# Kernel tuning notes

Measured on AMD Instinct MI355X. Metric: run time of the kernel, lower is better.

Reference implementation:

```python
import jax, jax.numpy as jnp
import numpy as np

D_MODEL = 1024
NUM_HEADS = 16
HEAD_DIM = D_MODEL // NUM_HEADS


def setup_inputs() -> dict:
    key = jax.random.key(0)
    ks = jax.random.split(key, 11)
    B, S = 2, 2048
    s = 1.0 / np.sqrt(D_MODEL)
    inp = {
        'q': jax.random.normal(ks[0], (B, S, D_MODEL), jnp.float32),
        'k': jax.random.normal(ks[1], (B, S, D_MODEL), jnp.float32),
        'v': jax.random.normal(ks[2], (B, S, D_MODEL), jnp.float32),
        'wq': jax.random.normal(ks[3], (D_MODEL, D_MODEL), jnp.float32) * s,
        'bq': jnp.zeros((D_MODEL,), jnp.float32),
        'wk': jax.random.normal(ks[4], (D_MODEL, D_MODEL), jnp.float32) * s,
        'bk': jnp.zeros((D_MODEL,), jnp.float32),
        'wv': jax.random.normal(ks[5], (D_MODEL, D_MODEL), jnp.float32) * s,
        'bv': jnp.zeros((D_MODEL,), jnp.float32),
        'wo': jax.random.normal(ks[6], (D_MODEL, D_MODEL), jnp.float32) * s,
        'bo': jnp.zeros((D_MODEL,), jnp.float32),
    }
    return inp


def _split_heads(x, B):
    # [B, S, D] -> [B, H, S, Hd]
    return x.reshape(B, -1, NUM_HEADS, HEAD_DIM).transpose(0, 2, 1, 3)


def reference(q, k, v, wq, bq, wk, bk, wv, bv, wo, bo):
    B = q.shape[0]
    qh = _split_heads(q @ wq + bq, B)
    kh = _split_heads(k @ wk + bk, B)
    vh = _split_heads(v @ wv + bv, B)
    scale = 1.0 / np.sqrt(HEAD_DIM).astype(np.float32)
    # [B, H, Sq, Sk]
    scores = jnp.einsum('bhqd,bhkd->bhqk', qh, kh) * scale
    probs = jax.nn.softmax(scores, axis=-1)
    out = jnp.einsum('bhqk,bhkd->bhqd', probs, vh)  # [B, H, Sq, Hd]
    out = out.transpose(0, 2, 1, 3).reshape(B, -1, D_MODEL)
    return out @ wo + bo
```

## Files before the change

kernel.cpp:

```cpp
#include <hip/hip_runtime.h>

typedef unsigned short u16;
typedef __bf16 bf16x8 __attribute__((ext_vector_type(8)));
typedef float    f32x4 __attribute__((ext_vector_type(4)));
typedef float   f32x16 __attribute__((ext_vector_type(16)));
typedef u16      u16x8 __attribute__((ext_vector_type(8)));
typedef u16      u16x4 __attribute__((ext_vector_type(4)));
typedef unsigned uint4v __attribute__((ext_vector_type(4)));

#define DM 1024
#define SQ 2048
#define HD 64
#define QSCALE 0.18033688f

#define SWZ8(row, ch) ((((ch) ^ ((row) & 7) ^ ((row) >> 3)) & 7))

__device__ __forceinline__ u16 f2bf(float f) {
    unsigned u = __builtin_bit_cast(unsigned, f);
    u += 0x7FFFu + ((u >> 16) & 1u);
    return (u16)(u >> 16);
}

__device__ __forceinline__ bf16x8 ldsbf(const u16* p) {
    return __builtin_bit_cast(bf16x8, *(const u16x8*)p);
}

__device__ __forceinline__ unsigned cvtpk(float a, float b) {
    unsigned r;
    asm("v_cvt_pk_bf16_f32 %0, %1, %2" : "=v"(r) : "v"(a), "v"(b));
    return r;
}

__device__ __forceinline__ void swap32(unsigned &a, unsigned &b) {
    asm volatile("v_permlane32_swap_b32 %0, %1" : "+v"(a), "+v"(b));
}

typedef __attribute__((address_space(3))) unsigned lds_u32_t;
typedef __attribute__((address_space(1))) const unsigned glob_u32_t;
__device__ __forceinline__ void gl_lds16(const u16* g, u16* l) {
    __builtin_amdgcn_global_load_lds((glob_u32_t*)g, (lds_u32_t*)l, 16, 0, 0);
}

__global__ __launch_bounds__(256) void convert_kernel(
    const float* __restrict__ q, const float* __restrict__ k,
    const float* __restrict__ v,
    u16* __restrict__ Qc, u16* __restrict__ Kc, u16* __restrict__ Vc)
{
    const int which = blockIdx.x >> 11;
    const float* src = (which==0) ? q : (which==1) ? k : v;
    u16* dst         = (which==0) ? Qc : (which==1) ? Kc : Vc;
    const int off = ((blockIdx.x & 2047) << 11) + threadIdx.x * 8;
    f32x4 x0 = *(const f32x4*)&src[off];
    f32x4 x1 = *(const f32x4*)&src[off + 4];
    u16x8 u;
#pragma unroll
    for (int e = 0; e < 4; ++e) { u[e] = f2bf(x0[e]); u[e+4] = f2bf(x1[e]); }
    *(u16x8*)&dst[off] = u;
}

__global__ __launch_bounds__(256) void wtrans_kernel(
    const float* __restrict__ w0, const float* __restrict__ w1,
    const float* __restrict__ w2, const float* __restrict__ w3,
    u16* __restrict__ t0, u16* __restrict__ t1,
    u16* __restrict__ t2, u16* __restrict__ t3)
{
    __shared__ float tile[32][33];
    const int z = blockIdx.z;
    const float* W = (z==0) ? w0 : (z==1) ? w1 : (z==2) ? w2 : w3;
    u16* T        = (z==0) ? t0 : (z==1) ? t1 : (z==2) ? t2 : t3;
    const float sc = (z==0) ? QSCALE : 1.0f;
    const int tx = threadIdx.x & 31, ty = threadIdx.x >> 5;
    const int n0 = blockIdx.x * 32, k0 = blockIdx.y * 32;
#pragma unroll
    for (int i = 0; i < 4; ++i)
        tile[ty + 8*i][tx] = W[(size_t)(k0 + ty + 8*i)*DM + n0 + tx];
    __syncthreads();
#pragma unroll
    for (int i = 0; i < 4; ++i)
        T[(size_t)(n0 + ty + 8*i)*DM + k0 + tx] = f2bf(tile[tx][ty + 8*i] * sc);
}

template<bool OF32, bool VTLAST>
__global__ __launch_bounds__(256) void gemm_kernel(
    const u16* __restrict__ a0, const u16* __restrict__ a1, const u16* __restrict__ a2,
    const u16* __restrict__ w0, const u16* __restrict__ w1, const u16* __restrict__ w2,
    const float* __restrict__ bi0, const float* __restrict__ bi1, const float* __restrict__ bi2,
    void* __restrict__ o0, void* __restrict__ o1, void* __restrict__ o2,
    float bscale0)
{
    __shared__ __align__(16) u16 As[128*64];
    __shared__ __align__(16) u16 Bs[128*64];

    const int cpx  = gridDim.x >> 3;
    const int wgid = (blockIdx.x & 7) * cpx + (blockIdx.x >> 3);
    const int z   = wgid >> 8;
    const int rem = wgid & 255;
    const int by  = rem >> 3, bx = rem & 7;

    const u16*  Ap  = (z==0) ? a0 : (z==1) ? a1 : a2;
    const u16*  Wp  = (z==0) ? w0 : (z==1) ? w1 : w2;
    const float* Bp = (z==0) ? bi0 : (z==1) ? bi1 : bi2;
    void* Op        = (z==0) ? o0 : (z==1) ? o1 : o2;
    const float bsc = (z==0) ? bscale0 : 1.0f;

    const int tid  = threadIdx.x;
    const int lane = tid & 63;
    const int wv   = tid >> 6;
    const int m0 = by * 128;
    const int n0 = bx * 128;
    const int wr = (wv >> 1) * 64;
    const int wc = (wv & 1) * 64;
    const int g  = lane >> 4;
    const int mm = lane & 15;

    const int l8  = lane >> 3;
    const int chs = (lane & 7) ^ l8;
    const int lrow = wv*8 + l8;

    const f32x4 zero4 = {0.f, 0.f, 0.f, 0.f};
    f32x4 acc[4][4];
#pragma unroll
    for (int i = 0; i < 4; ++i)
#pragma unroll
        for (int j = 0; j < 4; ++j) acc[i][j] = zero4;

    for (int kt = 0; kt < 16; ++kt) {
        const int k0 = kt * 64;
#pragma unroll
        for (int i = 0; i < 4; ++i) {
            const int row = i*32 + lrow;
            gl_lds16(&Ap[(size_t)(m0+row)*DM + k0 + chs*8], &As[(i*32 + wv*8)*64]);
            gl_lds16(&Wp[(size_t)(n0+row)*DM + k0 + chs*8], &Bs[(i*32 + wv*8)*64]);
        }
        __syncthreads();
#pragma unroll
        for (int ks = 0; ks < 2; ++ks) {
            bf16x8 af[4], bfr[4];
#pragma unroll
            for (int rt = 0; rt < 4; ++rt) {
                const int row = wr + rt*16 + mm;
                const int ch  = ks*4 + g;
                af[rt] = ldsbf(&As[row*64 + ((ch ^ (row & 7)) << 3)]);
            }
#pragma unroll
            for (int ct = 0; ct < 4; ++ct) {
                const int row = wc + ct*16 + mm;
                const int ch  = ks*4 + g;
                bfr[ct] = ldsbf(&Bs[row*64 + ((ch ^ (row & 7)) << 3)]);
            }
            __builtin_amdgcn_s_setprio(1);
#pragma unroll
            for (int rt = 0; rt < 4; ++rt)
#pragma unroll
                for (int ct = 0; ct < 4; ++ct)
                    acc[rt][ct] = __builtin_amdgcn_mfma_f32_16x16x32_bf16(
                        af[rt], bfr[ct], acc[rt][ct], 0, 0, 0);
            __builtin_amdgcn_s_setprio(0);
        }
        __syncthreads();
    }
    if (VTLAST && z == 2) {
#pragma unroll
        for (int ct = 0; ct < 4; ++ct) {
            const int col = n0 + wc + ct*16 + mm;
            const float bv = Bp[col] * bsc;
#pragma unroll
            for (int rt = 0; rt < 4; ++rt) {
                const int row0 = m0 + wr + rt*16 + g*4;
                const int bb = row0 >> 11, s = row0 & (SQ-1);
                u16x4 pk;
#pragma unroll
                for (int r = 0; r < 4; ++r) pk[r] = f2bf(acc[rt][ct][r] + bv);
                *(u16x4*)&((u16*)Op)[(size_t)(bb*DM + col)*SQ + s] = pk;
            }
        }
    } else {
#pragma unroll
        for (int ct = 0; ct < 4; ++ct) {
            const int col = n0 + wc + ct*16 + mm;
            const float bv = Bp[col] * bsc;
#pragma unroll
            for (int rt = 0; rt < 4; ++rt) {
#pragma unroll
                for (int r = 0; r < 4; ++r) {
                    const int row = m0 + wr + rt*16 + g*4 + r;
                    const float vv = acc[rt][ct][r] + bv;
                    if (OF32) ((float*)Op)[(size_t)row*DM + col] = vv;
                    else      ((u16*) Op)[(size_t)row*DM + col] = f2bf(vv);
                }
            }
        }
    }
}

__global__ __launch_bounds__(256) void attn_kernel(
    const u16* __restrict__ Q, const u16* __restrict__ K,
    const u16* __restrict__ Vt, u16* __restrict__ Z)
{
    __shared__ __align__(16) u16 Kl[2][64*64];
    __shared__ __align__(16) u16 Vl[2][64*64];

    const int tid  = threadIdx.x;
    const int lane = tid & 63;
    const int wid  = tid >> 6;
    const int c    = lane & 31;
    const int hi   = lane >> 5;
    const int l8   = lane >> 3;
    const int c8l  = lane & 7;
    const int rb   = wid*8 + l8;

    const int wg = (blockIdx.x & 7) * 64 + (blockIdx.x >> 3);
    const int qt = wg & 15;
    const int hb = wg >> 4;
    const int h  = hb & 15;
    const int b  = hb >> 4;
    const int q0 = qt * 128;

    const size_t kbase = (size_t)(b*SQ)*DM + h*HD;
    const size_t vbase = (size_t)((b*16 + h)*HD)*SQ;

    bf16x8 qf[4];
    {
        const size_t qoff = (size_t)(b*SQ + q0 + wid*32 + c)*DM + h*HD + hi*8;
#pragma unroll
        for (int ks = 0; ks < 4; ++ks)
            qf[ks] = ldsbf(&Q[qoff + ks*16]);
    }

    f32x16 oacc[2];
#pragma unroll
    for (int dt = 0; dt < 2; ++dt)
#pragma unroll
        for (int r = 0; r < 16; ++r) oacc[dt][r] = 0.f;
    f32x16 z16;
#pragma unroll
    for (int r = 0; r < 16; ++r) z16[r] = 0.f;
    float lsp[4] = {0.f, 0.f, 0.f, 0.f};

    auto stage = [&](int tt, int buf) {
#pragma unroll
        for (int p = 0; p < 2; ++p) {
            const int row = p*32 + rb;
            const int ch  = (c8l ^ (row & 7) ^ (row >> 3)) & 7;
            gl_lds16(&K [kbase + (size_t)(tt*64 + row)*DM + ch*8],
                     &Kl[buf][(p*32 + wid*8)*64]);
            gl_lds16(&Vt[vbase + (size_t)row*SQ + tt*64 + ch*8],
                     &Vl[buf][(p*32 + wid*8)*64]);
        }
    };

    stage(0, 0);

    for (int t = 0; t < SQ/64; ++t) {
        const int cur = t & 1;
        __syncthreads();
        if (t + 1 < SQ/64) stage(t+1, cur^1);

        f32x16 pacc[2];
        __builtin_amdgcn_s_setprio(1);
#pragma unroll
        for (int kt = 0; kt < 2; ++kt) {
            const int row = kt*32 + c;
            bf16x8 kf = ldsbf(&Kl[cur][row*64 + (SWZ8(row, hi) << 3)]);
            pacc[kt] = __builtin_amdgcn_mfma_f32_32x32x16_bf16(kf, qf[0], z16, 0, 0, 0);
        }
#pragma unroll
        for (int ks = 1; ks < 4; ++ks) {
#pragma unroll
            for (int kt = 0; kt < 2; ++kt) {
                const int row = kt*32 + c;
                const int ch  = ks*2 + hi;
                bf16x8 kf = ldsbf(&Kl[cur][row*64 + (SWZ8(row, ch) << 3)]);
                pacc[kt] = __builtin_amdgcn_mfma_f32_32x32x16_bf16(kf, qf[ks], pacc[kt], 0, 0, 0);
            }
        }
        __builtin_amdgcn_s_setprio(0);

#pragma unroll
        for (int kt = 0; kt < 2; ++kt)
#pragma unroll
            for (int r = 0; r < 16; ++r) {
                const float e = __builtin_amdgcn_exp2f(pacc[kt][r]);
                pacc[kt][r] = e;
                lsp[r & 3] += e;
            }

        bf16x8 pa[4];
#pragma unroll
        for (int kt = 0; kt < 2; ++kt)
#pragma unroll
            for (int k2 = 0; k2 < 2; ++k2) {
                const int bs = k2*8;
                unsigned u = cvtpk(pacc[kt][bs+0], pacc[kt][bs+1]);
                unsigned v = cvtpk(pacc[kt][bs+2], pacc[kt][bs+3]);
                unsigned w = cvtpk(pacc[kt][bs+4], pacc[kt][bs+5]);
                unsigned x = cvtpk(pacc[kt][bs+6], pacc[kt][bs+7]);
                swap32(u, w);
                swap32(v, x);
                uint4v fr = {u, v, w, x};
                pa[kt*2 + k2] = __builtin_bit_cast(bf16x8, fr);
            }

        __builtin_amdgcn_s_setprio(1);
#pragma unroll
        for (int kp = 0; kp < 4; ++kp) {
#pragma unroll
            for (int dt = 0; dt < 2; ++dt) {
                const int d  = dt*32 + c;
                const int ch = kp*2 + hi;
                bf16x8 vf = ldsbf(&Vl[cur][d*64 + (SWZ8(d, ch) << 3)]);
                oacc[dt] = __builtin_amdgcn_mfma_f32_32x32x16_bf16(pa[kp], vf, oacc[dt], 0, 0, 0);
            }
        }
        __builtin_amdgcn_s_setprio(0);
    }

    float lsum = (lsp[0] + lsp[1]) + (lsp[2] + lsp[3]);
    lsum += __shfl_xor(lsum, 32, 64);
    const float linv = 1.f / lsum;
    float linvr[16];
#pragma unroll
    for (int r = 0; r < 16; ++r)
        linvr[r] = __shfl(linv, (r & 3) + 8*(r >> 2) + 4*hi, 64);

#pragma unroll
    for (int dt = 0; dt < 2; ++dt)
#pragma unroll
        for (int r = 0; r < 16; ++r) {
            const int qrl = (r & 3) + 8*(r >> 2) + 4*hi;
            const size_t row = (size_t)(b*SQ + q0 + wid*32 + qrl);
            Z[row*DM + h*HD + dt*32 + c] = f2bf(oacc[dt][r] * linvr[r]);
        }
}

extern "C" void kernel_launch(void* const* d_in, const int* in_sizes, int n_in,
                              void* d_out, int out_size, void* d_ws, size_t ws_size,
                              hipStream_t stream)
{
    const float* q  = (const float*)d_in[0];
    const float* k  = (const float*)d_in[1];
    const float* v  = (const float*)d_in[2];
    const float* wq = (const float*)d_in[3];
    const float* bq = (const float*)d_in[4];
    const float* wk = (const float*)d_in[5];
    const float* bk = (const float*)d_in[6];
    const float* wv = (const float*)d_in[7];
    const float* bv = (const float*)d_in[8];
    const float* wo = (const float*)d_in[9];
    const float* bo = (const float*)d_in[10];
    float* out = (float*)d_out;

    char* ws = (char*)d_ws;
    u16* Qc  = (u16*)(ws);
    u16* Kc  = (u16*)(ws + 8388608);
    u16* Vc  = (u16*)(ws + 16777216);
    u16* Qb  = (u16*)(ws + 25165824);
    u16* Kb  = (u16*)(ws + 33554432);
    u16* VtB = (u16*)(ws + 41943040);
    u16* WtQ = (u16*)(ws + 50331648);
    u16* WtK = (u16*)(ws + 52428800);
    u16* WtV = (u16*)(ws + 54525952);
    u16* WtO = (u16*)(ws + 56623104);
    u16* Zb  = Qc;

    wtrans_kernel<<<dim3(32, 32, 4), 256, 0, stream>>>(
        wq, wk, wv, wo, WtQ, WtK, WtV, WtO);

    convert_kernel<<<dim3(3*2048), 256, 0, stream>>>(q, k, v, Qc, Kc, Vc);

    gemm_kernel<false, true><<<dim3(768), 256, 0, stream>>>(
        Qc, Kc, Vc, WtQ, WtK, WtV, bq, bk, bv,
        (void*)Qb, (void*)Kb, (void*)VtB, QSCALE);

    attn_kernel<<<dim3(512), 256, 0, stream>>>(Qb, Kb, VtB, Zb);

    gemm_kernel<true, false><<<dim3(256), 256, 0, stream>>>(
        Zb, Zb, Zb, WtO, WtO, WtO, bo, bo, bo,
        (void*)out, (void*)out, (void*)out, 1.0f);
}
```

Baseline: 135.0 us.

## Fuse fp32-to-bf16 input conversion into QKV GEMM and enlarge attention blocks

Removes the separate convert kernel. The QKV projection GEMM now loads fp32 activations directly, converts them with packed bf16 conversion instructions, and writes them swizzled into LDS, which avoids a full round trip of the bf16 intermediates through memory. The attention kernel moves to 512-thread blocks covering 256 queries each. Its K/V staging switches from async global-to-LDS loads to register prefetch that is stored to LDS after compute. The A-tile loads in the GEMM become synchronous register loads, which may lose the async overlap, and the larger attention blocks halve the grid size.

```diff
diff --git a/kernel.cpp b/kernel.cpp
--- a/kernel.cpp
+++ b/kernel.cpp
@@ -39,23 +39,6 @@
 typedef __attribute__((address_space(1))) const unsigned glob_u32_t;
 __device__ __forceinline__ void gl_lds16(const u16* g, u16* l) {
     __builtin_amdgcn_global_load_lds((glob_u32_t*)g, (lds_u32_t*)l, 16, 0, 0);
-}
-
-__global__ __launch_bounds__(256) void convert_kernel(
-    const float* __restrict__ q, const float* __restrict__ k,
-    const float* __restrict__ v,
-    u16* __restrict__ Qc, u16* __restrict__ Kc, u16* __restrict__ Vc)
-{
-    const int which = blockIdx.x >> 11;
-    const float* src = (which==0) ? q : (which==1) ? k : v;
-    u16* dst         = (which==0) ? Qc : (which==1) ? Kc : Vc;
-    const int off = ((blockIdx.x & 2047) << 11) + threadIdx.x * 8;
-    f32x4 x0 = *(const f32x4*)&src[off];
-    f32x4 x1 = *(const f32x4*)&src[off + 4];
-    u16x8 u;
-#pragma unroll
-    for (int e = 0; e < 4; ++e) { u[e] = f2bf(x0[e]); u[e+4] = f2bf(x1[e]); }
-    *(u16x8*)&dst[off] = u;
 }
 
 __global__ __launch_bounds__(256) void wtrans_kernel(
@@ -80,9 +63,9 @@
         T[(size_t)(n0 + ty + 8*i)*DM + k0 + tx] = f2bf(tile[tx][ty + 8*i] * sc);
 }
 
-template<bool OF32, bool VTLAST>
+template<bool AFP32, bool OF32, bool VTLAST>
 __global__ __launch_bounds__(256) void gemm_kernel(
-    const u16* __restrict__ a0, const u16* __restrict__ a1, const u16* __restrict__ a2,
+    const void* __restrict__ a0, const void* __restrict__ a1, const void* __restrict__ a2,
     const u16* __restrict__ w0, const u16* __restrict__ w1, const u16* __restrict__ w2,
     const float* __restrict__ bi0, const float* __restrict__ bi1, const float* __restrict__ bi2,
     void* __restrict__ o0, void* __restrict__ o1, void* __restrict__ o2,
@@ -97,7 +80,7 @@
     const int rem = wgid & 255;
     const int by  = rem >> 3, bx = rem & 7;
 
-    const u16*  Ap  = (z==0) ? a0 : (z==1) ? a1 : a2;
+    const void* Ap  = (z==0) ? a0 : (z==1) ? a1 : a2;
     const u16*  Wp  = (z==0) ? w0 : (z==1) ? w1 : w2;
     const float* Bp = (z==0) ? bi0 : (z==1) ? bi1 : bi2;
     void* Op        = (z==0) ? o0 : (z==1) ? o1 : o2;
@@ -116,6 +99,8 @@
     const int l8  = lane >> 3;
     const int chs = (lane & 7) ^ l8;
     const int lrow = wv*8 + l8;
+    const int srow = tid >> 3;
+    const int c8   = tid & 7;
 
     const f32x4 zero4 = {0.f, 0.f, 0.f, 0.f};
     f32x4 acc[4][4];
@@ -129,8 +114,29 @@
 #pragma unroll
         for (int i = 0; i < 4; ++i) {
             const int row = i*32 + lrow;
-            gl_lds16(&Ap[(size_t)(m0+row)*DM + k0 + chs*8], &As[(i*32 + wv*8)*64]);
             gl_lds16(&Wp[(size_t)(n0+row)*DM + k0 + chs*8], &Bs[(i*32 + wv*8)*64]);
+        }
+        if (AFP32) {
+#pragma unroll
+            for (int p = 0; p < 4; ++p) {
+                const int row = p*32 + srow;
+                const float* src = (const float*)Ap + (size_t)(m0+row)*DM + k0 + c8*8;
+                f32x4 x0 = *(const f32x4*)src;
+                f32x4 x1 = *(const f32x4*)(src + 4);
+                uint4v w;
+                w[0] = cvtpk(x0[0], x0[1]);
+                w[1] = cvtpk(x0[2], x0[3]);
+                w[2] = cvtpk(x1[0], x1[1]);
+                w[3] = cvtpk(x1[2], x1[3]);
+                *(uint4v*)&As[row*64 + ((c8 ^ (row & 7)) << 3)] = w;
+            }
+        } else {
+#pragma unroll
+            for (int i = 0; i < 4; ++i) {
+                const int row = i*32 + lrow;
+                gl_lds16(&((const u16*)Ap)[(size_t)(m0+row)*DM + k0 + chs*8],
+                         &As[(i*32 + wv*8)*64]);
+            }
         }
         __syncthreads();
 #pragma unroll
@@ -193,7 +199,7 @@
     }
 }
 
-__global__ __launch_bounds__(256) void attn_kernel(
+__global__ __launch_bounds__(512) void attn_kernel(
     const u16* __restrict__ Q, const u16* __restrict__ K,
     const u16* __restrict__ Vt, u16* __restrict__ Z)
 {
@@ -205,16 +211,15 @@
     const int wid  = tid >> 6;
     const int c    = lane & 31;
     const int hi   = lane >> 5;
-    const int l8   = lane >> 3;
-    const int c8l  = lane & 7;
-    const int rb   = wid*8 + l8;
-
-    const int wg = (blockIdx.x & 7) * 64 + (blockIdx.x >> 3);
-    const int qt = wg & 15;
-    const int hb = wg >> 4;
+    const int srow = tid >> 3;
+    const int c8   = tid & 7;
+
+    const int wg = (blockIdx.x & 7) * 32 + (blockIdx.x >> 3);
+    const int qt = wg & 7;
+    const int hb = wg >> 3;
     const int h  = hb & 15;
     const int b  = hb >> 4;
-    const int q0 = qt * 128;
+    const int q0 = qt * 256;
 
     const size_t kbase = (size_t)(b*SQ)*DM + h*HD;
     const size_t vbase = (size_t)((b*16 + h)*HD)*SQ;
@@ -237,24 +242,19 @@
     for (int r = 0; r < 16; ++r) z16[r] = 0.f;
     float lsp[4] = {0.f, 0.f, 0.f, 0.f};
 
-    auto stage = [&](int tt, int buf) {
-#pragma unroll
-        for (int p = 0; p < 2; ++p) {
-            const int row = p*32 + rb;
-            const int ch  = (c8l ^ (row & 7) ^ (row >> 3)) & 7;
-            gl_lds16(&K [kbase + (size_t)(tt*64 + row)*DM + ch*8],
-                     &Kl[buf][(p*32 + wid*8)*64]);
-            gl_lds16(&Vt[vbase + (size_t)row*SQ + tt*64 + ch*8],
-                     &Vl[buf][(p*32 + wid*8)*64]);
-        }
-    };
-
-    stage(0, 0);
+    const int stw = srow*64 + (SWZ8(srow, c8) << 3);
+    u16x8 kreg = *(const u16x8*)&K [kbase + (size_t)srow*DM + c8*8];
+    u16x8 vreg = *(const u16x8*)&Vt[vbase + (size_t)srow*SQ + c8*8];
+    *(u16x8*)&Kl[0][stw] = kreg;
+    *(u16x8*)&Vl[0][stw] = vreg;
 
     for (int t = 0; t < SQ/64; ++t) {
         const int cur = t & 1;
         __syncthreads();
-        if (t + 1 < SQ/64) stage(t+1, cur^1);
+        if (t + 1 < SQ/64) {
+            kreg = *(const u16x8*)&K [kbase + (size_t)((t+1)*64 + srow)*DM + c8*8];
+            vreg = *(const u16x8*)&Vt[vbase + (size_t)srow*SQ + (t+1)*64 + c8*8];
+        }
 
         f32x16 pacc[2];
         __builtin_amdgcn_s_setprio(1);
@@ -313,6 +313,11 @@
             }
         }
         __builtin_amdgcn_s_setprio(0);
+
+        if (t + 1 < SQ/64) {
+            *(u16x8*)&Kl[cur^1][stw] = kreg;
+            *(u16x8*)&Vl[cur^1][stw] = vreg;
+        }
     }
 
     float lsum = (lsp[0] + lsp[1]) + (lsp[2] + lsp[3]);
@@ -351,30 +356,27 @@
     float* out = (float*)d_out;
 
     char* ws = (char*)d_ws;
-    u16* Qc  = (u16*)(ws);
-    u16* Kc  = (u16*)(ws + 8388608);
-    u16* Vc  = (u16*)(ws + 16777216);
-    u16* Qb  = (u16*)(ws + 25165824);
-    u16* Kb  = (u16*)(ws + 33554432);
-    u16* VtB = (u16*)(ws + 41943040);
-    u16* WtQ = (u16*)(ws + 50331648);
-    u16* WtK = (u16*)(ws + 52428800);
-    u16* WtV = (u16*)(ws + 54525952);
-    u16* WtO = (u16*)(ws + 56623104);
-    u16* Zb  = Qc;
+    u16* Qb  = (u16*)(ws);
+    u16* Kb  = (u16*)(ws + 8388608);
+    u16* VtB = (u16*)(ws + 16777216);
+    u16* Zb  = (u16*)(ws + 25165824);
+    u16* WtQ = (u16*)(ws + 33554432);
+    u16* WtK = (u16*)(ws + 35651584);
+    u16* WtV = (u16*)(ws + 37748736);
+    u16* WtO = (u16*)(ws + 39845888);
 
     wtrans_kernel<<<dim3(32, 32, 4), 256, 0, stream>>>(
         wq, wk, wv, wo, WtQ, WtK, WtV, WtO);
 
-    convert_kernel<<<dim3(3*2048), 256, 0, stream>>>(q, k, v, Qc, Kc, Vc);
-
-    gemm_kernel<false, true><<<dim3(768), 256, 0, stream>>>(
-        Qc, Kc, Vc, WtQ, WtK, WtV, bq, bk, bv,
+    gemm_kernel<true, false, true><<<dim3(768), 256, 0, stream>>>(
+        (const void*)q, (const void*)k, (const void*)v,
+        WtQ, WtK, WtV, bq, bk, bv,
         (void*)Qb, (void*)Kb, (void*)VtB, QSCALE);
 
-    attn_kernel<<<dim3(512), 256, 0, stream>>>(Qb, Kb, VtB, Zb);
-
-    gemm_kernel<true, false><<<dim3(256), 256, 0, stream>>>(
-        Zb, Zb, Zb, WtO, WtO, WtO, bo, bo, bo,
+    attn_kernel<<<dim3(256), 512, 0, stream>>>(Qb, Kb, VtB, Zb);
+
+    gemm_kernel<false, true, false><<<dim3(256), 256, 0, stream>>>(
+        (const void*)Zb, (const void*)Zb, (const void*)Zb,
+        WtO, WtO, WtO, bo, bo, bo,
         (void*)out, (void*)out, (void*)out, 1.0f);
 }
```

Result: faster. 123.9 us (-8.2%).

## Double-buffer GEMM K-tiles and enlarge attention blocks with register-staged K/V loads

Applied to the files above, without the earlier changes.

The GEMM now uses two LDS buffers with 32-wide K tiles, prefetching the next tile while MFMAs run on the current one, which removes one barrier per iteration. The attention kernel moves to 512-thread blocks, each covering 256 queries, so every K/V tile loaded into LDS is reused across twice as many query rows. K/V staging changes from direct global-to-LDS loads to global-to-register loads that are written to LDS after the compute. This adds register pressure and halves the number of attention blocks, which may reduce how well the CUs are filled.

```diff
diff --git a/kernel.cpp b/kernel.cpp
--- a/kernel.cpp
+++ b/kernel.cpp
@@ -14,6 +14,7 @@
 #define QSCALE 0.18033688f
 
 #define SWZ8(row, ch) ((((ch) ^ ((row) & 7) ^ ((row) >> 3)) & 7))
+#define SWZ4(row) (((row) >> 1) & 3)
 
 __device__ __forceinline__ u16 f2bf(float f) {
     unsigned u = __builtin_bit_cast(unsigned, f);
@@ -88,8 +89,8 @@
     void* __restrict__ o0, void* __restrict__ o1, void* __restrict__ o2,
     float bscale0)
 {
-    __shared__ __align__(16) u16 As[128*64];
-    __shared__ __align__(16) u16 Bs[128*64];
+    __shared__ __align__(16) u16 As[2][128*32];
+    __shared__ __align__(16) u16 Bs[2][128*32];
 
     const int cpx  = gridDim.x >> 3;
     const int wgid = (blockIdx.x & 7) * cpx + (blockIdx.x >> 3);
@@ -113,9 +114,8 @@
     const int g  = lane >> 4;
     const int mm = lane & 15;
 
-    const int l8  = lane >> 3;
-    const int chs = (lane & 7) ^ l8;
-    const int lrow = wv*8 + l8;
+    const int l4r = lane >> 2;
+    const int sl  = lane & 3;
 
     const f32x4 zero4 = {0.f, 0.f, 0.f, 0.f};
     f32x4 acc[4][4];
@@ -124,41 +124,57 @@
 #pragma unroll
         for (int j = 0; j < 4; ++j) acc[i][j] = zero4;
 
-    for (int kt = 0; kt < 16; ++kt) {
-        const int k0 = kt * 64;
-#pragma unroll
-        for (int i = 0; i < 4; ++i) {
-            const int row = i*32 + lrow;
-            gl_lds16(&Ap[(size_t)(m0+row)*DM + k0 + chs*8], &As[(i*32 + wv*8)*64]);
-            gl_lds16(&Wp[(size_t)(n0+row)*DM + k0 + chs*8], &Bs[(i*32 + wv*8)*64]);
-        }
-        __syncthreads();
-#pragma unroll
-        for (int ks = 0; ks < 2; ++ks) {
-            bf16x8 af[4], bfr[4];
-#pragma unroll
-            for (int rt = 0; rt < 4; ++rt) {
-                const int row = wr + rt*16 + mm;
-                const int ch  = ks*4 + g;
-                af[rt] = ldsbf(&As[row*64 + ((ch ^ (row & 7)) << 3)]);
-            }
-#pragma unroll
-            for (int ct = 0; ct < 4; ++ct) {
-                const int row = wc + ct*16 + mm;
-                const int ch  = ks*4 + g;
-                bfr[ct] = ldsbf(&Bs[row*64 + ((ch ^ (row & 7)) << 3)]);
-            }
-            __builtin_amdgcn_s_setprio(1);
-#pragma unroll
-            for (int rt = 0; rt < 4; ++rt)
-#pragma unroll
-                for (int ct = 0; ct < 4; ++ct)
-                    acc[rt][ct] = __builtin_amdgcn_mfma_f32_16x16x32_bf16(
-                        af[rt], bfr[ct], acc[rt][ct], 0, 0, 0);
-            __builtin_amdgcn_s_setprio(0);
-        }
-        __syncthreads();
+    auto stageA = [&](int kt, int buf) {
+#pragma unroll
+        for (int i = 0; i < 2; ++i) {
+            const int row = i*64 + wv*16 + l4r;
+            const int ch  = sl ^ SWZ4(row);
+            gl_lds16(&Ap[(size_t)(m0+row)*DM + kt*32 + ch*8],
+                     &As[buf][(i*64 + wv*16)*32]);
+        }
+    };
+    auto stageW = [&](int kt, int buf) {
+#pragma unroll
+        for (int i = 0; i < 2; ++i) {
+            const int row = i*64 + wv*16 + l4r;
+            const int ch  = sl ^ SWZ4(row);
+            gl_lds16(&Wp[(size_t)(n0+row)*DM + kt*32 + ch*8],
+                     &Bs[buf][(i*64 + wv*16)*32]);
+        }
+    };
+
+    stageA(0, 0);
+    stageW(0, 0);
+    __syncthreads();
+
+    for (int kt = 0; kt < 32; ++kt) {
+        const int cur = kt & 1;
+        if (kt < 31) {
+            stageA(kt + 1, cur ^ 1);
+            stageW(kt + 1, cur ^ 1);
+        }
+        bf16x8 af[4], bfr[4];
+#pragma unroll
+        for (int rt = 0; rt < 4; ++rt) {
+            const int row = wr + rt*16 + mm;
+            af[rt] = ldsbf(&As[cur][row*32 + ((g ^ SWZ4(row)) << 3)]);
+        }
+#pragma unroll
+        for (int ct = 0; ct < 4; ++ct) {
+            const int row = wc + ct*16 + mm;
+            bfr[ct] = ldsbf(&Bs[cur][row*32 + ((g ^ SWZ4(row)) << 3)]);
+        }
+        __builtin_amdgcn_s_setprio(1);
+#pragma unroll
+        for (int rt = 0; rt < 4; ++rt)
+#pragma unroll
+            for (int ct = 0; ct < 4; ++ct)
+                acc[rt][ct] = __builtin_amdgcn_mfma_f32_16x16x32_bf16(
+                    af[rt], bfr[ct], acc[rt][ct], 0, 0, 0);
+        __builtin_amdgcn_s_setprio(0);
+        if (kt < 31) __syncthreads();
     }
+
     if (VTLAST && z == 2) {
 #pragma unroll
         for (int ct = 0; ct < 4; ++ct) {
@@ -193,7 +209,7 @@
     }
 }
 
-__global__ __launch_bounds__(256) void attn_kernel(
+__global__ __launch_bounds__(512) void attn_kernel(
     const u16* __restrict__ Q, const u16* __restrict__ K,
     const u16* __restrict__ Vt, u16* __restrict__ Z)
 {
@@ -205,16 +221,15 @@
     const int wid  = tid >> 6;
     const int c    = lane & 31;
     const int hi   = lane >> 5;
-    const int l8   = lane >> 3;
-    const int c8l  = lane & 7;
-    const int rb   = wid*8 + l8;
-
-    const int wg = (blockIdx.x & 7) * 64 + (blockIdx.x >> 3);
-    const int qt = wg & 15;
-    const int hb = wg >> 4;
+    const int srow = tid >> 3;
+    const int c8   = tid & 7;
+
+    const int wg = (blockIdx.x & 7) * 32 + (blockIdx.x >> 3);
+    const int qt = wg & 7;
+    const int hb = wg >> 3;
     const int h  = hb & 15;
     const int b  = hb >> 4;
-    const int q0 = qt * 128;
+    const int q0 = qt * 256;
 
     const size_t kbase = (size_t)(b*SQ)*DM + h*HD;
     const size_t vbase = (size_t)((b*16 + h)*HD)*SQ;
@@ -237,24 +252,19 @@
     for (int r = 0; r < 16; ++r) z16[r] = 0.f;
     float lsp[4] = {0.f, 0.f, 0.f, 0.f};
 
-    auto stage = [&](int tt, int buf) {
-#pragma unroll
-        for (int p = 0; p < 2; ++p) {
-            const int row = p*32 + rb;
-            const int ch  = (c8l ^ (row & 7) ^ (row >> 3)) & 7;
-            gl_lds16(&K [kbase + (size_t)(tt*64 + row)*DM + ch*8],
-                     &Kl[buf][(p*32 + wid*8)*64]);
-            gl_lds16(&Vt[vbase + (size_t)row*SQ + tt*64 + ch*8],
-                     &Vl[buf][(p*32 + wid*8)*64]);
-        }
-    };
-
-    stage(0, 0);
+    const int stw = srow*64 + (SWZ8(srow, c8) << 3);
+    u16x8 kreg = *(const u16x8*)&K [kbase + (size_t)srow*DM + c8*8];
+    u16x8 vreg = *(const u16x8*)&Vt[vbase + (size_t)srow*SQ + c8*8];
+    *(u16x8*)&Kl[0][stw] = kreg;
+    *(u16x8*)&Vl[0][stw] = vreg;
 
     for (int t = 0; t < SQ/64; ++t) {
         const int cur = t & 1;
         __syncthreads();
-        if (t + 1 < SQ/64) stage(t+1, cur^1);
+        if (t + 1 < SQ/64) {
+            kreg = *(const u16x8*)&K [kbase + (size_t)((t+1)*64 + srow)*DM + c8*8];
+            vreg = *(const u16x8*)&Vt[vbase + (size_t)srow*SQ + (t+1)*64 + c8*8];
+        }
 
         f32x16 pacc[2];
         __builtin_amdgcn_s_setprio(1);
@@ -313,6 +323,11 @@
             }
         }
         __builtin_amdgcn_s_setprio(0);
+
+        if (t + 1 < SQ/64) {
+            *(u16x8*)&Kl[cur^1][stw] = kreg;
+            *(u16x8*)&Vl[cur^1][stw] = vreg;
+        }
     }
 
     float lsum = (lsp[0] + lsp[1]) + (lsp[2] + lsp[3]);
@@ -372,7 +387,7 @@
         Qc, Kc, Vc, WtQ, WtK, WtV, bq, bk, bv,
         (void*)Qb, (void*)Kb, (void*)VtB, QSCALE);
 
-    attn_kernel<<<dim3(512), 256, 0, stream>>>(Qb, Kb, VtB, Zb);
+    attn_kernel<<<dim3(256), 512, 0, stream>>>(Qb, Kb, VtB, Zb);
 
     gemm_kernel<true, false><<<dim3(256), 256, 0, stream>>>(
         Zb, Zb, Zb, WtO, WtO, WtO, bo, bo, bo,
```

Measured after the change: 135.9 us. About the same (+0.6%).
